# Kernel optimization log

Hardware: AMD Instinct MI355X
Metric: run time of the kernel (lower is better)

Reference implementation:

```python
import jax, jax.numpy as jnp
import numpy as np

D_MODEL = 256
NUM_HEADS = 8
HEAD_DIM = D_MODEL // NUM_HEADS


def setup_inputs() -> dict:
    key = jax.random.key(0)
    ks = jax.random.split(key, 16)
    B, C, H, W = 2, D_MODEL, 64, 64
    s = 0.02
    inp = {
        "query_feat": jax.random.normal(ks[0], (B, C, H, W), jnp.float32),
        "lateral_feat": jax.random.normal(ks[1], (B, C, H, W), jnp.float32),
        # 1x1 convs == per-pixel linear layers: weight (out, in), bias (out,)
        "Wq": jax.random.normal(ks[2], (C, C), jnp.float32) * s,
        "bq": jnp.zeros((C,), jnp.float32),
        "Wk": jax.random.normal(ks[3], (C, C), jnp.float32) * s,
        "bk": jnp.zeros((C,), jnp.float32),
        "Wv": jax.random.normal(ks[4], (C, C), jnp.float32) * s,
        "bv": jnp.zeros((C,), jnp.float32),
        "Wo": jax.random.normal(ks[5], (C, C), jnp.float32) * s,
        "bo": jnp.zeros((C,), jnp.float32),
        "W1": jax.random.normal(ks[6], (4 * C, C), jnp.float32) * s,
        "b1": jnp.zeros((4 * C,), jnp.float32),
        "W2": jax.random.normal(ks[7], (C, 4 * C), jnp.float32) * s,
        "b2": jnp.zeros((C,), jnp.float32),
    }
    return inp


def reference(query_feat, lateral_feat, Wq, bq, Wk, bk, Wv, bv, Wo, bo, W1, b1, W2, b2):
    B, C, H, W = query_feat.shape
    N = H * W
    h, d = NUM_HEADS, HEAD_DIM
    scale = d ** -0.5

    # (B,C,H,W) -> (B,N,C) tokens
    xq = query_feat.reshape(B, C, N).transpose(0, 2, 1)
    xl = lateral_feat.reshape(B, C, N).transpose(0, 2, 1)

    # 1x1-conv projections = dense per-token linear
    Q = (xq @ Wq.T + bq).reshape(B, N, h, d).transpose(0, 2, 1, 3)  # (B,h,N,d)
    K = (xl @ Wk.T + bk).reshape(B, N, h, d).transpose(0, 2, 1, 3)
    V = (xl @ Wv.T + bv).reshape(B, N, h, d).transpose(0, 2, 1, 3)

    scores = jnp.einsum("bhqd,bhkd->bhqk", Q, K) * scale  # (B,h,N,N)
    attn = jax.nn.softmax(scores, axis=-1)  # dropout = identity at inference
    out = jnp.einsum("bhqk,bhkd->bhqd", attn, V)  # (B,h,N,d)

    out = out.transpose(0, 2, 1, 3).reshape(B, N, C)  # (B,N,C)
    out = out @ Wo.T + bo
    out = out.transpose(0, 2, 1).reshape(B, C, H, W)
    out = out + query_feat  # residual

    # MLP on channels (1x1 convs + exact GELU)
    t = out.reshape(B, C, N).transpose(0, 2, 1)  # (B,N,C)
    hdn = jax.nn.gelu(t @ W1.T + b1, approximate=False)  # (B,N,4C)
    mlp = (hdn @ W2.T + b2).transpose(0, 2, 1).reshape(B, C, H, W)
    return out + mlp
```

## Files before the change

### kernel.cpp

```cpp
#include <hip/hip_runtime.h>
#include <math.h>

namespace {

constexpr int kB  = 2;
constexpr int kC  = 256;
constexpr int kN  = 4096;
constexpr int kHD = 32;
constexpr int kC4 = 1024;

typedef __attribute__((ext_vector_type(8))) short bf16x8;
typedef __attribute__((ext_vector_type(4))) float f32x4;
typedef __attribute__((ext_vector_type(16))) float f32x16;

__device__ __forceinline__ float gelu_exact(float x) {
  return 0.5f * x * (1.0f + erff(x * 0.70710678118654752f));
}

__device__ __forceinline__ unsigned short f2bf(float x) {
  unsigned u = __builtin_bit_cast(unsigned, x);
  u += 0x7FFFu + ((u >> 16) & 1u);
  return (unsigned short)(u >> 16);
}

__device__ __forceinline__ float bf2f(unsigned short us) {
  return __builtin_bit_cast(float, (unsigned)us << 16);
}

__device__ __forceinline__ float exp2_hw(float x) {
#if __has_builtin(__builtin_amdgcn_exp2f)
  return __builtin_amdgcn_exp2f(x);
#else
  float r;
  asm("v_exp_f32 %0, %1\n\ts_nop 1" : "=v"(r) : "v"(x));
  return r;
#endif
}

__device__ __forceinline__ unsigned cvt_pk_bf16(float lo, float hi) {
  unsigned r;
  asm("v_cvt_pk_bf16_f32 %0, %1, %2" : "=v"(r) : "v"(lo), "v"(hi));
  return r;
}

__global__ __launch_bounds__(256)
void convert_all(const float* __restrict__ qfeat, const float* __restrict__ lfeat,
                 const float* __restrict__ Wq, const float* __restrict__ Wk,
                 const float* __restrict__ Wv, const float* __restrict__ Wo,
                 const float* __restrict__ W1, const float* __restrict__ W2,
                 unsigned short* __restrict__ qtok, unsigned short* __restrict__ ltok,
                 unsigned short* __restrict__ wbf)
{
  __shared__ float Lds[32][36];
  const int z = blockIdx.z;
  const int t = threadIdx.x;
  if (z < 4) {
    const float* src = (z < kB) ? qfeat : lfeat;
    unsigned short* dst = (z < kB) ? qtok : ltok;
    const int b = z & 1;
    src += (size_t)b * kC * kN;
    dst += (size_t)b * kN * kC;
    const int n0 = blockIdx.x * 32, c0 = blockIdx.y * 32;
    const int r = t >> 3, q4 = (t & 7) * 4;
    {
      const float4 v = *(const float4*)&src[(size_t)(c0 + r) * kN + n0 + q4];
      Lds[r][q4 + 0] = v.x; Lds[r][q4 + 1] = v.y; Lds[r][q4 + 2] = v.z; Lds[r][q4 + 3] = v.w;
    }
    __syncthreads();
    ushort4 p;
    p.x = f2bf(Lds[q4 + 0][r]); p.y = f2bf(Lds[q4 + 1][r]);
    p.z = f2bf(Lds[q4 + 2][r]); p.w = f2bf(Lds[q4 + 3][r]);
    *(ushort4*)&dst[(size_t)(n0 + r) * kC + c0 + q4] = p;
  } else {
    const int wi = blockIdx.y * 128 + blockIdx.x;
    if (wi >= 768) return;
    const int i4 = wi * 1024 + t * 4;
    const float* s; int base;
    if      (i4 < 65536)  { s = Wq; base = 0; }
    else if (i4 < 131072) { s = Wk; base = 65536; }
    else if (i4 < 196608) { s = Wv; base = 131072; }
    else if (i4 < 262144) { s = Wo; base = 196608; }
    else if (i4 < 524288) { s = W1; base = 262144; }
    else                  { s = W2; base = 524288; }
    const float4 v = *(const float4*)&s[i4 - base];
    ushort4 p;
    p.x = f2bf(v.x); p.y = f2bf(v.y); p.z = f2bf(v.z); p.w = f2bf(v.w);
    *(ushort4*)&wbf[i4] = p;
  }
}

__global__ __launch_bounds__(256)
void gemm_qkv(const unsigned short* __restrict__ wbf,
              const unsigned short* __restrict__ qtok,
              const unsigned short* __restrict__ ltok,
              const float* __restrict__ bq, const float* __restrict__ bk,
              const float* __restrict__ bv,
              unsigned short* __restrict__ qout, unsigned short* __restrict__ kout,
              unsigned short* __restrict__ vout, float qscale)
{
  __shared__ unsigned short Wlds[2][64 * 64];
  __shared__ unsigned short Xlds[2][64 * 64];

  const int z = blockIdx.z;
  const bool isQ = blockIdx.y < 4;
  const int m0 = (isQ ? blockIdx.y : blockIdx.y - 4) * 64;
  const unsigned short* Wb = isQ ? wbf : (wbf + 65536);
  const unsigned short* Xt = (isQ ? qtok : ltok) + (size_t)z * kN * kC;

  const int t = threadIdx.x;
  const int w = t >> 6, l = t & 63;
  const int r = l & 15, g = l >> 4;
  const int wm = w >> 1, wn = w & 1;
  const int n0 = blockIdx.x * 64;

  const int rw = t >> 3;
  const int sw = (t & 7) ^ (rw & 7);
  const unsigned short* wsrc = Wb + (size_t)(m0 + rw) * kC + sw * 8;
  const unsigned short* xsrc = Xt + (size_t)(n0 + rw) * kC + sw * 8;

  f32x4 acc[2][2];
#pragma unroll
  for (int i = 0; i < 2; ++i)
#pragma unroll
    for (int j = 0; j < 2; ++j) acc[i][j] = {0.f, 0.f, 0.f, 0.f};

  bf16x8 wrg[2], xrg[2];
#pragma unroll
  for (int j = 0; j < 2; ++j) {
    wrg[j] = *(const bf16x8*)(wsrc + (size_t)(32 * j) * kC);
    xrg[j] = *(const bf16x8*)(xsrc + (size_t)(32 * j) * kC);
  }

  for (int it = 0; it < 4; ++it) {
    unsigned short* wl = &Wlds[it & 1][0];
    unsigned short* xl = &Xlds[it & 1][0];
    *(bf16x8*)((char*)wl + t * 16)         = wrg[0];
    *(bf16x8*)((char*)wl + (256 + t) * 16) = wrg[1];
    *(bf16x8*)((char*)xl + t * 16)         = xrg[0];
    *(bf16x8*)((char*)xl + (256 + t) * 16) = xrg[1];
    if (it + 1 < 4) {
      const int ko = (it + 1) * 64;
#pragma unroll
      for (int j = 0; j < 2; ++j) {
        wrg[j] = *(const bf16x8*)(wsrc + (size_t)(32 * j) * kC + ko);
        xrg[j] = *(const bf16x8*)(xsrc + (size_t)(32 * j) * kC + ko);
      }
    }
    __syncthreads();
#pragma unroll
    for (int kc = 0; kc < 2; ++kc) {
      const int sl = ((kc * 4 + g) ^ (r & 7)) * 16;
      bf16x8 a0 = *(const bf16x8*)((const char*)wl + (wm * 32 + r) * 128 + sl);
      bf16x8 a1 = *(const bf16x8*)((const char*)wl + (wm * 32 + 16 + r) * 128 + sl);
      bf16x8 b0 = *(const bf16x8*)((const char*)xl + (wn * 32 + r) * 128 + sl);
      bf16x8 b1 = *(const bf16x8*)((const char*)xl + (wn * 32 + 16 + r) * 128 + sl);
      acc[0][0] = __builtin_amdgcn_mfma_f32_16x16x32_bf16(a0, b0, acc[0][0], 0, 0, 0);
      acc[0][1] = __builtin_amdgcn_mfma_f32_16x16x32_bf16(a0, b1, acc[0][1], 0, 0, 0);
      acc[1][0] = __builtin_amdgcn_mfma_f32_16x16x32_bf16(a1, b0, acc[1][0], 0, 0, 0);
      acc[1][1] = __builtin_amdgcn_mfma_f32_16x16x32_bf16(a1, b1, acc[1][1], 0, 0, 0);
    }
  }

#pragma unroll
  for (int f = 0; f < 2; ++f) {
    const int mb = m0 + wm * 32 + f * 16 + 4 * g;
    const float* bp = isQ ? (bq + mb) : (mb < 256 ? (bk + mb) : (bv + mb - 256));
    const float4 b4 = *(const float4*)bp;
    const float os = isQ ? qscale : 1.0f;
#pragma unroll
    for (int fn = 0; fn < 2; ++fn) {
      const int n = n0 + wn * 32 + fn * 16 + r;
      float v[4];
      v[0] = (acc[f][fn][0] + b4.x) * os; v[1] = (acc[f][fn][1] + b4.y) * os;
      v[2] = (acc[f][fn][2] + b4.z) * os; v[3] = (acc[f][fn][3] + b4.w) * os;
      if (isQ) {
        unsigned short* Yt = qout + (size_t)z * kN * kC;
        ushort4 pk;
        pk.x = f2bf(v[0]); pk.y = f2bf(v[1]); pk.z = f2bf(v[2]); pk.w = f2bf(v[3]);
        *(ushort4*)&Yt[(size_t)n * kC + mb] = pk;
      } else if (mb < 256) {
        unsigned short* Yt = kout + (size_t)z * kN * kC;
        ushort4 pk;
        pk.x = f2bf(v[0]); pk.y = f2bf(v[1]); pk.z = f2bf(v[2]); pk.w = f2bf(v[3]);
        *(ushort4*)&Yt[(size_t)n * kC + mb] = pk;
      } else {
        unsigned short* Yc = vout + (size_t)z * kC * kN;
#pragma unroll
        for (int q = 0; q < 4; ++q) Yc[(size_t)(mb - 256 + q) * kN + n] = f2bf(v[q]);
      }
    }
  }
}

template <int EPI, bool GELU, bool RES>
__global__ __launch_bounds__(256)
void gemm_mfma(const unsigned short* __restrict__ Wbf,
               const unsigned short* __restrict__ Xtok,
               const float* __restrict__ bias, const float* __restrict__ res,
               void* __restrict__ Y1, void* __restrict__ Y2,
               int M, int Nn, int K, float oscale)
{
  __shared__ unsigned short Wlds[2][64 * 64];
  __shared__ unsigned short Xlds[2][64 * 64];

  const int z = blockIdx.z;
  Xtok += (size_t)z * Nn * K;

  const int t = threadIdx.x;
  const int w = t >> 6, l = t & 63;
  const int r = l & 15, g = l >> 4;
  const int wm = w >> 1, wn = w & 1;
  const int m0 = blockIdx.y * 64, n0 = blockIdx.x * 64;

  const int rw = t >> 3;
  const int sw = (t & 7) ^ (rw & 7);
  const unsigned short* wsrc = Wbf + (size_t)(m0 + rw) * K + sw * 8;
  const unsigned short* xsrc = Xtok + (size_t)(n0 + rw) * K + sw * 8;

  f32x4 acc[2][2];
#pragma unroll
  for (int i = 0; i < 2; ++i)
#pragma unroll
    for (int j = 0; j < 2; ++j) acc[i][j] = {0.f, 0.f, 0.f, 0.f};

  bf16x8 wrg[2], xrg[2];
#pragma unroll
  for (int j = 0; j < 2; ++j) {
    wrg[j] = *(const bf16x8*)(wsrc + (size_t)(32 * j) * K);
    xrg[j] = *(const bf16x8*)(xsrc + (size_t)(32 * j) * K);
  }

  const int nit = K >> 6;
  for (int it = 0; it < nit; ++it) {
    unsigned short* wl = &Wlds[it & 1][0];
    unsigned short* xl = &Xlds[it & 1][0];
    *(bf16x8*)((char*)wl + t * 16)         = wrg[0];
    *(bf16x8*)((char*)wl + (256 + t) * 16) = wrg[1];
    *(bf16x8*)((char*)xl + t * 16)         = xrg[0];
    *(bf16x8*)((char*)xl + (256 + t) * 16) = xrg[1];
    if (it + 1 < nit) {
      const int ko = (it + 1) * 64;
#pragma unroll
      for (int j = 0; j < 2; ++j) {
        wrg[j] = *(const bf16x8*)(wsrc + (size_t)(32 * j) * K + ko);
        xrg[j] = *(const bf16x8*)(xsrc + (size_t)(32 * j) * K + ko);
      }
    }
    __syncthreads();
#pragma unroll
    for (int kc = 0; kc < 2; ++kc) {
      const int sl = ((kc * 4 + g) ^ (r & 7)) * 16;
      bf16x8 a0 = *(const bf16x8*)((const char*)wl + (wm * 32 + r) * 128 + sl);
      bf16x8 a1 = *(const bf16x8*)((const char*)wl + (wm * 32 + 16 + r) * 128 + sl);
      bf16x8 b0 = *(const bf16x8*)((const char*)xl + (wn * 32 + r) * 128 + sl);
      bf16x8 b1 = *(const bf16x8*)((const char*)xl + (wn * 32 + 16 + r) * 128 + sl);
      acc[0][0] = __builtin_amdgcn_mfma_f32_16x16x32_bf16(a0, b0, acc[0][0], 0, 0, 0);
      acc[0][1] = __builtin_amdgcn_mfma_f32_16x16x32_bf16(a0, b1, acc[0][1], 0, 0, 0);
      acc[1][0] = __builtin_amdgcn_mfma_f32_16x16x32_bf16(a1, b0, acc[1][0], 0, 0, 0);
      acc[1][1] = __builtin_amdgcn_mfma_f32_16x16x32_bf16(a1, b1, acc[1][1], 0, 0, 0);
    }
  }

#pragma unroll
  for (int f = 0; f < 2; ++f) {
    const int mb = m0 + wm * 32 + f * 16 + 4 * g;
    const float4 b4 = *(const float4*)&bias[mb];
#pragma unroll
    for (int fn = 0; fn < 2; ++fn) {
      const int n = n0 + wn * 32 + fn * 16 + r;
      float v[4];
      v[0] = (acc[f][fn][0] + b4.x) * oscale; v[1] = (acc[f][fn][1] + b4.y) * oscale;
      v[2] = (acc[f][fn][2] + b4.z) * oscale; v[3] = (acc[f][fn][3] + b4.w) * oscale;
      if (GELU) {
#pragma unroll
        for (int q = 0; q < 4; ++q) v[q] = gelu_exact(v[q]);
      }
      if (RES) {
#pragma unroll
        for (int q = 0; q < 4; ++q)
          v[q] += res[(size_t)z * M * Nn + (size_t)(mb + q) * Nn + n];
      }
      if constexpr (EPI == 7) {
        const unsigned short* Rt = (const unsigned short*)Y2 + (size_t)z * Nn * M;
        const ushort4 rr = *(const ushort4*)&Rt[(size_t)n * M + mb];
        v[0] += bf2f(rr.x); v[1] += bf2f(rr.y); v[2] += bf2f(rr.z); v[3] += bf2f(rr.w);
      }
      if constexpr (EPI == 1 || EPI == 7) {
        unsigned short* Yt = (unsigned short*)Y1 + (size_t)z * Nn * M;
        ushort4 pk;
        pk.x = f2bf(v[0]); pk.y = f2bf(v[1]); pk.z = f2bf(v[2]); pk.w = f2bf(v[3]);
        *(ushort4*)&Yt[(size_t)n * M + mb] = pk;
      }
      if constexpr (EPI == 6) {
        float* Yf = (float*)Y1 + (size_t)z * M * Nn;
        const unsigned short* Rt = (const unsigned short*)Y2 + (size_t)z * Nn * M;
#pragma unroll
        for (int q = 0; q < 4; ++q)
          Yf[(size_t)(mb + q) * Nn + n] = v[q] + bf2f(Rt[(size_t)n * M + mb + q]);
      }
    }
  }
}

__global__ __launch_bounds__(512, 4)
void attn_mfma32(const unsigned short* __restrict__ Qbf,
                 const unsigned short* __restrict__ Kbf,
                 const unsigned short* __restrict__ Vbf,
                 unsigned short* __restrict__ Aout)
{
  __shared__ __attribute__((aligned(16))) char smem[32768];

  const int id = blockIdx.x;
  const int bh = id & 15;
  const int b = bh >> 3, hd = bh & 7;
  const int t = threadIdx.x;
  const int w = t >> 6, l = t & 63;
  const int r = l & 31, hi = l >> 5;
  const int qg = w >> 1, kh = w & 1;

  const unsigned short* Qb = Qbf + (size_t)b * kN * kC;
  const unsigned short* Kb = Kbf + (size_t)b * kN * kC;
  const unsigned short* Vb = Vbf + ((size_t)b * kC + hd * kHD) * kN;
  unsigned short* Ap = Aout + (size_t)b * kN * kC;

  const int q0 = (id >> 4) * 128 + qg * 32;

  const bf16x8 qf0 = *(const bf16x8*)&Qb[(size_t)(q0 + r) * kC + hd * kHD + hi * 8];
  const bf16x8 qf1 = *(const bf16x8*)&Qb[(size_t)(q0 + r) * kC + hd * kHD + 16 + hi * 8];

  const int tt = t & 255, th = t >> 8;
  const unsigned short* ksrc = Kb + (size_t)(th * 2048 + (tt >> 2)) * kC + hd * kHD + (tt & 3) * 8;
  const unsigned short* vsrc = Vb + (size_t)(tt >> 3) * kN + th * 2048 + (tt & 7) * 8;
  char* kdst = smem + th * 4096 + ((tt & 3) * 64 + ((tt >> 2) ^ (9 * (tt & 3)))) * 16;
  char* vdst = smem + 8192 + th * 4096 + ((tt & 7) * 32 + ((tt >> 3) ^ (tt & 7))) * 16;

  int koff[2][2], voff[2][2];
#pragma unroll
  for (int ds = 0; ds < 2; ++ds)
#pragma unroll
    for (int tile = 0; tile < 2; ++tile) {
      const int c = 2 * ds + hi;
      koff[ds][tile] = kh * 4096 + (c * 64 + tile * 32 + (r ^ (9 * c))) * 16;
    }
#pragma unroll
  for (int ktile = 0; ktile < 2; ++ktile)
#pragma unroll
    for (int kc = 0; kc < 2; ++kc) {
      const int c = ktile * 4 + kc * 2 + hi;
      voff[ktile][kc] = 8192 + kh * 4096 + (c * 32 + (r ^ c)) * 16;
    }

  const f32x16 ZV = {0.f};
  f32x16 oA = ZV, oB = ZV;
  float lsum = 0.f;

  bf16x8 krg = *(const bf16x8*)ksrc;
  bf16x8 vrg = *(const bf16x8*)vsrc;

  for (int it = 0; it < 32; ++it) {
    const int bo = (it & 1) << 14;
    *(bf16x8*)(kdst + bo) = krg;
    *(bf16x8*)(vdst + bo) = vrg;
    if (it + 1 < 32) {
      krg = *(const bf16x8*)(ksrc + (size_t)(it + 1) * 64 * kC);
      vrg = *(const bf16x8*)(vsrc + (it + 1) * 64);
    }
    __syncthreads();

    bf16x8 ka00 = *(const bf16x8*)(smem + bo + koff[0][0]);
    bf16x8 ka10 = *(const bf16x8*)(smem + bo + koff[1][0]);
    bf16x8 ka01 = *(const bf16x8*)(smem + bo + koff[0][1]);
    bf16x8 ka11 = *(const bf16x8*)(smem + bo + koff[1][1]);
    __builtin_amdgcn_s_setprio(1);
    f32x16 s0 = __builtin_amdgcn_mfma_f32_32x32x16_bf16(ka00, qf0, ZV, 0, 0, 0);
    s0        = __builtin_amdgcn_mfma_f32_32x32x16_bf16(ka10, qf1, s0, 0, 0, 0);
    f32x16 s1 = __builtin_amdgcn_mfma_f32_32x32x16_bf16(ka01, qf0, ZV, 0, 0, 0);
    s1        = __builtin_amdgcn_mfma_f32_32x32x16_bf16(ka11, qf1, s1, 0, 0, 0);
    __builtin_amdgcn_s_setprio(0);

#pragma unroll
    for (int ktile = 0; ktile < 2; ++ktile) {
      const f32x16& sv = ktile ? s1 : s0;
      float pe[16];
#pragma unroll
      for (int j = 0; j < 16; ++j) pe[j] = exp2_hw(sv[j]);
      lsum += (((pe[0] + pe[1]) + (pe[2] + pe[3])) + ((pe[4] + pe[5]) + (pe[6] + pe[7])))
            + (((pe[8] + pe[9]) + (pe[10] + pe[11])) + ((pe[12] + pe[13]) + (pe[14] + pe[15])));
      const unsigned c0 = cvt_pk_bf16(pe[0], pe[1]),   c1 = cvt_pk_bf16(pe[2], pe[3]);
      const unsigned c2 = cvt_pk_bf16(pe[4], pe[5]),   c3 = cvt_pk_bf16(pe[6], pe[7]);
      const unsigned c4 = cvt_pk_bf16(pe[8], pe[9]),   c5 = cvt_pk_bf16(pe[10], pe[11]);
      const unsigned c6 = cvt_pk_bf16(pe[12], pe[13]), c7 = cvt_pk_bf16(pe[14], pe[15]);
      auto a02 = __builtin_amdgcn_permlane32_swap(c0, c2, false, false);
      auto a13 = __builtin_amdgcn_permlane32_swap(c1, c3, false, false);
      auto a46 = __builtin_amdgcn_permlane32_swap(c4, c6, false, false);
      auto a57 = __builtin_amdgcn_permlane32_swap(c5, c7, false, false);
      union { unsigned u[4]; bf16x8 v; } p0, p1;
      p0.u[0] = a02[0]; p0.u[1] = a13[0]; p0.u[2] = a02[1]; p0.u[3] = a13[1];
      p1.u[0] = a46[0]; p1.u[1] = a57[0]; p1.u[2] = a46[1]; p1.u[3] = a57[1];
      bf16x8 vf0 = *(const bf16x8*)(smem + bo + voff[ktile][0]);
      bf16x8 vf1 = *(const bf16x8*)(smem + bo + voff[ktile][1]);
      __builtin_amdgcn_s_setprio(1);
      oA = __builtin_amdgcn_mfma_f32_32x32x16_bf16(vf0, p0.v, oA, 0, 0, 0);
      oB = __builtin_amdgcn_mfma_f32_32x32x16_bf16(vf1, p1.v, oB, 0, 0, 0);
      __builtin_amdgcn_s_setprio(0);
    }
  }

  {
    auto pr = __builtin_amdgcn_permlane32_swap(
        __builtin_bit_cast(unsigned, lsum), __builtin_bit_cast(unsigned, lsum), false, false);
    lsum = __builtin_bit_cast(float, (unsigned)pr[0]) + __builtin_bit_cast(float, (unsigned)pr[1]);
  }
  float oS[16];
#pragma unroll
  for (int j = 0; j < 16; ++j) oS[j] = oA[j] + oB[j];

  float* Scr = (float*)smem;
  __syncthreads();
  if (kh == 1) {
    float* S = Scr + ((size_t)qg * 64 + l) * 17;
#pragma unroll
    for (int j = 0; j < 16; ++j) S[j] = oS[j];
    S[16] = lsum;
  }
  __syncthreads();
  if (kh == 0) {
    const float* S = Scr + ((size_t)qg * 64 + l) * 17;
#pragma unroll
    for (int j = 0; j < 16; ++j) oS[j] += S[j];
    lsum += S[16];
    const float inv = 1.f / lsum;

    unsigned* T = (unsigned*)(Scr + (size_t)qg * 64 * 17);
#pragma unroll
    for (int p = 0; p < 8; ++p) {
      const int r2 = 4 * (p >> 1) + 2 * hi + (p & 1);
      T[r2 * 33 + r] = cvt_pk_bf16(oS[2 * p] * inv, oS[2 * p + 1] * inv);
    }
    unsigned v[8];
#pragma unroll
    for (int j = 0; j < 8; ++j) v[j] = T[(8 * hi + j) * 33 + r];
    unsigned short* outp = Ap + (size_t)(q0 + r) * kC + hd * kHD + hi * 16;
    uint4 w0{v[0], v[1], v[2], v[3]}, w1{v[4], v[5], v[6], v[7]};
    *(uint4*)outp = w0;
    *(uint4*)(outp + 8) = w1;
  }
}

}

extern "C" void kernel_launch(void* const* d_in, const int* in_sizes, int n_in,
                              void* d_out, int out_size, void* d_ws, size_t ws_size,
                              hipStream_t stream)
{
  const float* qfeat = (const float*)d_in[0];
  const float* lfeat = (const float*)d_in[1];
  const float* Wq = (const float*)d_in[2];
  const float* bq = (const float*)d_in[3];
  const float* Wk = (const float*)d_in[4];
  const float* bk = (const float*)d_in[5];
  const float* Wv = (const float*)d_in[6];
  const float* bv = (const float*)d_in[7];
  const float* Wo = (const float*)d_in[8];
  const float* bo = (const float*)d_in[9];
  const float* W1 = (const float*)d_in[10];
  const float* b1 = (const float*)d_in[11];
  const float* W2 = (const float*)d_in[12];
  const float* b2 = (const float*)d_in[13];
  float* out = (float*)d_out;
  (void)in_sizes; (void)n_in; (void)out_size; (void)ws_size;

  constexpr float kScaleLog2e = 0.25506970f;

  const size_t bcn = (size_t)kB * kC * kN;
  unsigned short* qtok   = (unsigned short*)d_ws;
  unsigned short* ltok   = qtok + bcn;
  unsigned short* wbf    = ltok + bcn;
  unsigned short* qbf    = wbf + 786432;
  unsigned short* kbf    = qbf + bcn;
  unsigned short* vbf    = kbf + bcn;
  unsigned short* atok   = vbf + bcn;
  unsigned short* owstok = atok + bcn;
  unsigned short* h1tok  = owstok + bcn;

  dim3 blk(256);

  convert_all<<<dim3(128, 8, 5), blk, 0, stream>>>(
      qfeat, lfeat, Wq, Wk, Wv, Wo, W1, W2, qtok, ltok, wbf);

  gemm_qkv<<<dim3(64, 12, 2), blk, 0, stream>>>(
      wbf, qtok, ltok, bq, bk, bv, qbf, kbf, vbf, kScaleLog2e);

  attn_mfma32<<<dim3(512), dim3(512), 0, stream>>>(qbf, kbf, vbf, atok);

  gemm_mfma<7, false, false><<<dim3(64, 4, 2), blk, 0, stream>>>(
      wbf + 196608, atok, bo, nullptr, owstok, qtok, kC, kN, kC, 1.0f);
  gemm_mfma<1, true, false><<<dim3(64, 16, 2), blk, 0, stream>>>(
      wbf + 262144, owstok, b1, nullptr, h1tok, nullptr, kC4, kN, kC, 1.0f);
  gemm_mfma<6, false, false><<<dim3(64, 4, 2), blk, 0, stream>>>(
      wbf + 524288, h1tok, b2, nullptr, out, owstok, kC, kN, kC4, 1.0f);
}
```

Baseline: 100.0 us.

## Split attention over key halves with separate combine kernel

Attention is split into two key-range partitions per query block, doubling the block count. Each block writes unnormalized fp32 partial outputs and row sums to workspace. A new combine kernel sums the partials, normalizes, and writes bf16 tokens. This aims to improve GPU occupancy and load balance, at the cost of extra global memory traffic and an additional kernel launch.

After: 105.4 us. +5.3%, slower.

```diff
diff --git a/kernel.cpp b/kernel.cpp
--- a/kernel.cpp
+++ b/kernel.cpp
@@ -303,15 +303,17 @@
 }
 
 __global__ __launch_bounds__(512, 4)
-void attn_mfma32(const unsigned short* __restrict__ Qbf,
-                 const unsigned short* __restrict__ Kbf,
-                 const unsigned short* __restrict__ Vbf,
-                 unsigned short* __restrict__ Aout)
+void attn_part(const unsigned short* __restrict__ Qbf,
+               const unsigned short* __restrict__ Kbf,
+               const unsigned short* __restrict__ Vbf,
+               float* __restrict__ partO, float* __restrict__ partL)
 {
   __shared__ __attribute__((aligned(16))) char smem[32768];
 
   const int id = blockIdx.x;
   const int bh = id & 15;
+  const int part = (id >> 4) & 1;
+  const int qblk = id >> 5;
   const int b = bh >> 3, hd = bh & 7;
   const int t = threadIdx.x;
   const int w = t >> 6, l = t & 63;
@@ -321,16 +323,16 @@
   const unsigned short* Qb = Qbf + (size_t)b * kN * kC;
   const unsigned short* Kb = Kbf + (size_t)b * kN * kC;
   const unsigned short* Vb = Vbf + ((size_t)b * kC + hd * kHD) * kN;
-  unsigned short* Ap = Aout + (size_t)b * kN * kC;
-
-  const int q0 = (id >> 4) * 128 + qg * 32;
+
+  const int q0 = qblk * 128 + qg * 32;
 
   const bf16x8 qf0 = *(const bf16x8*)&Qb[(size_t)(q0 + r) * kC + hd * kHD + hi * 8];
   const bf16x8 qf1 = *(const bf16x8*)&Qb[(size_t)(q0 + r) * kC + hd * kHD + 16 + hi * 8];
 
   const int tt = t & 255, th = t >> 8;
-  const unsigned short* ksrc = Kb + (size_t)(th * 2048 + (tt >> 2)) * kC + hd * kHD + (tt & 3) * 8;
-  const unsigned short* vsrc = Vb + (size_t)(tt >> 3) * kN + th * 2048 + (tt & 7) * 8;
+  const int kb0 = part * 2048 + th * 1024;
+  const unsigned short* ksrc = Kb + (size_t)(kb0 + (tt >> 2)) * kC + hd * kHD + (tt & 3) * 8;
+  const unsigned short* vsrc = Vb + (size_t)(tt >> 3) * kN + kb0 + (tt & 7) * 8;
   char* kdst = smem + th * 4096 + ((tt & 3) * 64 + ((tt >> 2) ^ (9 * (tt & 3)))) * 16;
   char* vdst = smem + 8192 + th * 4096 + ((tt & 7) * 32 + ((tt >> 3) ^ (tt & 7))) * 16;
 
@@ -357,11 +359,11 @@
   bf16x8 krg = *(const bf16x8*)ksrc;
   bf16x8 vrg = *(const bf16x8*)vsrc;
 
-  for (int it = 0; it < 32; ++it) {
+  for (int it = 0; it < 16; ++it) {
     const int bo = (it & 1) << 14;
     *(bf16x8*)(kdst + bo) = krg;
     *(bf16x8*)(vdst + bo) = vrg;
-    if (it + 1 < 32) {
+    if (it + 1 < 16) {
       krg = *(const bf16x8*)(ksrc + (size_t)(it + 1) * 64 * kC);
       vrg = *(const bf16x8*)(vsrc + (it + 1) * 64);
     }
@@ -429,21 +431,61 @@
 #pragma unroll
     for (int j = 0; j < 16; ++j) oS[j] += S[j];
     lsum += S[16];
-    const float inv = 1.f / lsum;
-
-    unsigned* T = (unsigned*)(Scr + (size_t)qg * 64 * 17);
-#pragma unroll
-    for (int p = 0; p < 8; ++p) {
-      const int r2 = 4 * (p >> 1) + 2 * hi + (p & 1);
-      T[r2 * 33 + r] = cvt_pk_bf16(oS[2 * p] * inv, oS[2 * p + 1] * inv);
-    }
-    unsigned v[8];
-#pragma unroll
-    for (int j = 0; j < 8; ++j) v[j] = T[(8 * hi + j) * 33 + r];
-    unsigned short* outp = Ap + (size_t)(q0 + r) * kC + hd * kHD + hi * 16;
-    uint4 w0{v[0], v[1], v[2], v[3]}, w1{v[4], v[5], v[6], v[7]};
-    *(uint4*)outp = w0;
-    *(uint4*)(outp + 8) = w1;
+
+    float* PO = partO + (((size_t)part * kB + b) * 8 + hd) * 32 * (size_t)kN;
+#pragma unroll
+    for (int j = 0; j < 16; ++j) {
+      const int d = (j & 3) + 8 * (j >> 2) + 4 * hi;
+      PO[(size_t)d * kN + q0 + r] = oS[j];
+    }
+    if (hi == 0)
+      partL[(((size_t)part * kB + b) * 8 + hd) * (size_t)kN + q0 + r] = lsum;
+  }
+}
+
+__global__ __launch_bounds__(256)
+void attn_combine(const float* __restrict__ partO, const float* __restrict__ partL,
+                  unsigned short* __restrict__ atok)
+{
+  __shared__ float Lds[32][72];
+  const int b = blockIdx.z, hd = blockIdx.y, q0 = blockIdx.x * 64;
+  const int t = threadIdx.x;
+
+  const size_t o0 = (((size_t)0 * kB + b) * 8 + hd) * 32 * (size_t)kN;
+  const size_t o1 = (((size_t)1 * kB + b) * 8 + hd) * 32 * (size_t)kN;
+  const size_t l0 = (((size_t)0 * kB + b) * 8 + hd) * (size_t)kN;
+  const size_t l1 = (((size_t)1 * kB + b) * 8 + hd) * (size_t)kN;
+
+  const int d = t >> 3, q8 = (t & 7) * 8;
+  {
+    const float4 a0 = *(const float4*)&partO[o0 + (size_t)d * kN + q0 + q8];
+    const float4 a1 = *(const float4*)&partO[o0 + (size_t)d * kN + q0 + q8 + 4];
+    const float4 b0 = *(const float4*)&partO[o1 + (size_t)d * kN + q0 + q8];
+    const float4 b1 = *(const float4*)&partO[o1 + (size_t)d * kN + q0 + q8 + 4];
+    const float4 la0 = *(const float4*)&partL[l0 + q0 + q8];
+    const float4 la1 = *(const float4*)&partL[l0 + q0 + q8 + 4];
+    const float4 lb0 = *(const float4*)&partL[l1 + q0 + q8];
+    const float4 lb1 = *(const float4*)&partL[l1 + q0 + q8 + 4];
+    Lds[d][q8 + 0] = (a0.x + b0.x) / (la0.x + lb0.x);
+    Lds[d][q8 + 1] = (a0.y + b0.y) / (la0.y + lb0.y);
+    Lds[d][q8 + 2] = (a0.z + b0.z) / (la0.z + lb0.z);
+    Lds[d][q8 + 3] = (a0.w + b0.w) / (la0.w + lb0.w);
+    Lds[d][q8 + 4] = (a1.x + b1.x) / (la1.x + lb1.x);
+    Lds[d][q8 + 5] = (a1.y + b1.y) / (la1.y + lb1.y);
+    Lds[d][q8 + 6] = (a1.z + b1.z) / (la1.z + lb1.z);
+    Lds[d][q8 + 7] = (a1.w + b1.w) / (la1.w + lb1.w);
+  }
+  __syncthreads();
+  {
+    const int q = t >> 2, c8 = (t & 3) * 8;
+    ushort4 p0, p1;
+    p0.x = f2bf(Lds[c8 + 0][q]); p0.y = f2bf(Lds[c8 + 1][q]);
+    p0.z = f2bf(Lds[c8 + 2][q]); p0.w = f2bf(Lds[c8 + 3][q]);
+    p1.x = f2bf(Lds[c8 + 4][q]); p1.y = f2bf(Lds[c8 + 5][q]);
+    p1.z = f2bf(Lds[c8 + 6][q]); p1.w = f2bf(Lds[c8 + 7][q]);
+    unsigned short* outp = atok + ((size_t)b * kN + q0 + q) * kC + hd * kHD + c8;
+    *(ushort4*)outp = p0;
+    *(ushort4*)(outp + 4) = p1;
   }
 }
 
@@ -482,6 +524,8 @@
   unsigned short* atok   = vbf + bcn;
   unsigned short* owstok = atok + bcn;
   unsigned short* h1tok  = owstok + bcn;
+  float*          partO  = (float*)(h1tok + (size_t)kB * kC4 * kN);
+  float*          partL  = partO + (size_t)2 * kB * 8 * 32 * kN;
 
   dim3 blk(256);
 
@@ -491,7 +535,8 @@
   gemm_qkv<<<dim3(64, 12, 2), blk, 0, stream>>>(
       wbf, qtok, ltok, bq, bk, bv, qbf, kbf, vbf, kScaleLog2e);
 
-  attn_mfma32<<<dim3(512), dim3(512), 0, stream>>>(qbf, kbf, vbf, atok);
+  attn_part<<<dim3(1024), dim3(512), 0, stream>>>(qbf, kbf, vbf, partO, partL);
+  attn_combine<<<dim3(64, 8, 2), blk, 0, stream>>>(partO, partL, atok);
 
   gemm_mfma<7, false, false><<<dim3(64, 4, 2), blk, 0, stream>>>(
       wbf + 196608, atok, bo, nullptr, owstok, qtok, kC, kN, kC, 1.0f);
```

## Process two K/V tiles per barrier in attention loop with larger LDS

Applied to the files above, without the earlier changes.

The attention kernel now stages two 64-key K/V tiles per iteration into a doubled 64KB shared buffer, halving the number of __syncthreads barriers and issuing eight independent QK MFMAs back-to-back before the softmax/PV work. The aim is to amortize barrier and load latency and raise MFMA instruction-level parallelism. In exchange, LDS use doubles and the occupancy hint of 4 blocks is dropped, so fewer blocks may be resident per CU and register pressure rises.

Result: slower. 104.0 us (+4.0%).

```diff
diff --git a/kernel.cpp b/kernel.cpp
--- a/kernel.cpp
+++ b/kernel.cpp
@@ -302,13 +302,13 @@
   }
 }
 
-__global__ __launch_bounds__(512, 4)
+__global__ __launch_bounds__(512)
 void attn_mfma32(const unsigned short* __restrict__ Qbf,
                  const unsigned short* __restrict__ Kbf,
                  const unsigned short* __restrict__ Vbf,
                  unsigned short* __restrict__ Aout)
 {
-  __shared__ __attribute__((aligned(16))) char smem[32768];
+  __shared__ __attribute__((aligned(16))) char smem[65536];
 
   const int id = blockIdx.x;
   const int bh = id & 15;
@@ -354,33 +354,10 @@
   f32x16 oA = ZV, oB = ZV;
   float lsum = 0.f;
 
-  bf16x8 krg = *(const bf16x8*)ksrc;
-  bf16x8 vrg = *(const bf16x8*)vsrc;
-
-  for (int it = 0; it < 32; ++it) {
-    const int bo = (it & 1) << 14;
-    *(bf16x8*)(kdst + bo) = krg;
-    *(bf16x8*)(vdst + bo) = vrg;
-    if (it + 1 < 32) {
-      krg = *(const bf16x8*)(ksrc + (size_t)(it + 1) * 64 * kC);
-      vrg = *(const bf16x8*)(vsrc + (it + 1) * 64);
-    }
-    __syncthreads();
-
-    bf16x8 ka00 = *(const bf16x8*)(smem + bo + koff[0][0]);
-    bf16x8 ka10 = *(const bf16x8*)(smem + bo + koff[1][0]);
-    bf16x8 ka01 = *(const bf16x8*)(smem + bo + koff[0][1]);
-    bf16x8 ka11 = *(const bf16x8*)(smem + bo + koff[1][1]);
-    __builtin_amdgcn_s_setprio(1);
-    f32x16 s0 = __builtin_amdgcn_mfma_f32_32x32x16_bf16(ka00, qf0, ZV, 0, 0, 0);
-    s0        = __builtin_amdgcn_mfma_f32_32x32x16_bf16(ka10, qf1, s0, 0, 0, 0);
-    f32x16 s1 = __builtin_amdgcn_mfma_f32_32x32x16_bf16(ka01, qf0, ZV, 0, 0, 0);
-    s1        = __builtin_amdgcn_mfma_f32_32x32x16_bf16(ka11, qf1, s1, 0, 0, 0);
-    __builtin_amdgcn_s_setprio(0);
-
+  auto softmax_pv = [&](const f32x16& s0v, const f32x16& s1v, int vb) {
 #pragma unroll
     for (int ktile = 0; ktile < 2; ++ktile) {
-      const f32x16& sv = ktile ? s1 : s0;
+      const f32x16& sv = ktile ? s1v : s0v;
       float pe[16];
 #pragma unroll
       for (int j = 0; j < 16; ++j) pe[j] = exp2_hw(sv[j]);
@@ -397,13 +374,57 @@
       union { unsigned u[4]; bf16x8 v; } p0, p1;
       p0.u[0] = a02[0]; p0.u[1] = a13[0]; p0.u[2] = a02[1]; p0.u[3] = a13[1];
       p1.u[0] = a46[0]; p1.u[1] = a57[0]; p1.u[2] = a46[1]; p1.u[3] = a57[1];
-      bf16x8 vf0 = *(const bf16x8*)(smem + bo + voff[ktile][0]);
-      bf16x8 vf1 = *(const bf16x8*)(smem + bo + voff[ktile][1]);
+      bf16x8 vf0 = *(const bf16x8*)(smem + vb + voff[ktile][0]);
+      bf16x8 vf1 = *(const bf16x8*)(smem + vb + voff[ktile][1]);
       __builtin_amdgcn_s_setprio(1);
       oA = __builtin_amdgcn_mfma_f32_32x32x16_bf16(vf0, p0.v, oA, 0, 0, 0);
       oB = __builtin_amdgcn_mfma_f32_32x32x16_bf16(vf1, p1.v, oB, 0, 0, 0);
       __builtin_amdgcn_s_setprio(0);
     }
+  };
+
+  bf16x8 krgA = *(const bf16x8*)ksrc;
+  bf16x8 vrgA = *(const bf16x8*)vsrc;
+  bf16x8 krgB = *(const bf16x8*)(ksrc + (size_t)64 * kC);
+  bf16x8 vrgB = *(const bf16x8*)(vsrc + 64);
+
+  for (int rd = 0; rd < 16; ++rd) {
+    const int bo = (rd & 1) << 15;
+    *(bf16x8*)(kdst + bo) = krgA;
+    *(bf16x8*)(vdst + bo) = vrgA;
+    *(bf16x8*)(kdst + bo + 16384) = krgB;
+    *(bf16x8*)(vdst + bo + 16384) = vrgB;
+    if (rd + 1 < 16) {
+      const unsigned short* kn = ksrc + (size_t)(rd + 1) * 128 * kC;
+      const unsigned short* vn = vsrc + (rd + 1) * 128;
+      krgA = *(const bf16x8*)kn;
+      vrgA = *(const bf16x8*)vn;
+      krgB = *(const bf16x8*)(kn + (size_t)64 * kC);
+      vrgB = *(const bf16x8*)(vn + 64);
+    }
+    __syncthreads();
+
+    bf16x8 a00A = *(const bf16x8*)(smem + bo + koff[0][0]);
+    bf16x8 a10A = *(const bf16x8*)(smem + bo + koff[1][0]);
+    bf16x8 a01A = *(const bf16x8*)(smem + bo + koff[0][1]);
+    bf16x8 a11A = *(const bf16x8*)(smem + bo + koff[1][1]);
+    bf16x8 a00B = *(const bf16x8*)(smem + bo + 16384 + koff[0][0]);
+    bf16x8 a10B = *(const bf16x8*)(smem + bo + 16384 + koff[1][0]);
+    bf16x8 a01B = *(const bf16x8*)(smem + bo + 16384 + koff[0][1]);
+    bf16x8 a11B = *(const bf16x8*)(smem + bo + 16384 + koff[1][1]);
+    __builtin_amdgcn_s_setprio(1);
+    f32x16 sA0 = __builtin_amdgcn_mfma_f32_32x32x16_bf16(a00A, qf0, ZV, 0, 0, 0);
+    f32x16 sA1 = __builtin_amdgcn_mfma_f32_32x32x16_bf16(a01A, qf0, ZV, 0, 0, 0);
+    f32x16 sB0 = __builtin_amdgcn_mfma_f32_32x32x16_bf16(a00B, qf0, ZV, 0, 0, 0);
+    f32x16 sB1 = __builtin_amdgcn_mfma_f32_32x32x16_bf16(a01B, qf0, ZV, 0, 0, 0);
+    sA0 = __builtin_amdgcn_mfma_f32_32x32x16_bf16(a10A, qf1, sA0, 0, 0, 0);
+    sA1 = __builtin_amdgcn_mfma_f32_32x32x16_bf16(a11A, qf1, sA1, 0, 0, 0);
+    sB0 = __builtin_amdgcn_mfma_f32_32x32x16_bf16(a10B, qf1, sB0, 0, 0, 0);
+    sB1 = __builtin_amdgcn_mfma_f32_32x32x16_bf16(a11B, qf1, sB1, 0, 0, 0);
+    __builtin_amdgcn_s_setprio(0);
+
+    softmax_pv(sA0, sA1, bo);
+    softmax_pv(sB0, sB1, bo + 16384);
   }
 
   {
```
